# Performance work log

Measured on AMD Instinct MI355X. Metric: run time of the kernel, lower is better.

## Reference

```python
import jax, jax.numpy as jnp
import numpy as np

B, N_HIST, N_PRED = 32, 12, 12
N_NODE, INPUT_DIM, OUTPUT_DIM = 325, 2, 1
HIDDEN, N_RNN_LAYERS = 256, 2
EDGE_DIM, NODE_DIM, ORDER = 2, 64, 2
K = ORDER * EDGE_DIM + 1  # number of concat blocks per GraphConv


def setup_inputs() -> dict:
    key = jax.random.key(0)
    ks = iter(jax.random.split(key, 40))

    def rn(shape, s=0.05):
        return jax.random.normal(next(ks), shape, jnp.float32) * s

    L, H = N_RNN_LAYERS, HIDDEN
    d = {}
    d['inputs'] = jax.random.normal(next(ks), (B, N_HIST, N_NODE, INPUT_DIM), jnp.float32)
    d['vertexes'] = rn((N_NODE, NODE_DIM), 1.0)
    d['arcs_w0'] = rn((2 * NODE_DIM, 4 * NODE_DIM)); d['arcs_b0'] = jnp.zeros((4 * NODE_DIM,), jnp.float32)
    d['arcs_w1'] = rn((4 * NODE_DIM, 4 * NODE_DIM)); d['arcs_b1'] = jnp.zeros((4 * NODE_DIM,), jnp.float32)
    d['arcs_w2'] = rn((4 * NODE_DIM, EDGE_DIM)); d['arcs_b2'] = jnp.zeros((EDGE_DIM,), jnp.float32)
    d['enc_pre_w0'] = rn((K * INPUT_DIM, H)); d['enc_pre_b0'] = jnp.zeros((H,), jnp.float32)
    d['enc_pre_w1'] = rn((K * H, H)); d['enc_pre_b1'] = jnp.zeros((H,), jnp.float32)
    d['enc_wih'] = rn((L, 4 * H, H)); d['enc_whh'] = rn((L, 4 * H, H))
    d['enc_bih'] = jnp.zeros((L, 4 * H), jnp.float32); d['enc_bhh'] = jnp.zeros((L, 4 * H), jnp.float32)
    d['dec_pre_w0'] = rn((K * OUTPUT_DIM, H)); d['dec_pre_b0'] = jnp.zeros((H,), jnp.float32)
    d['dec_pre_w1'] = rn((K * H, H)); d['dec_pre_b1'] = jnp.zeros((H,), jnp.float32)
    d['dec_wih'] = rn((L, 4 * H, H)); d['dec_whh'] = rn((L, 4 * H, H))
    d['dec_bih'] = jnp.zeros((L, 4 * H), jnp.float32); d['dec_bhh'] = jnp.zeros((L, 4 * H), jnp.float32)
    d['dec_post_w0'] = rn((K * H, H)); d['dec_post_b0'] = jnp.zeros((H,), jnp.float32)
    d['dec_post_w1'] = rn((K * H, H)); d['dec_post_b1'] = jnp.zeros((H,), jnp.float32)
    d['proj_w'] = rn((H, OUTPUT_DIM)); d['proj_b'] = jnp.zeros((OUTPUT_DIM,), jnp.float32)
    return d


def _graph_conv(x, supports, w, b):
    out = [x]
    for e in range(supports.shape[0]):
        a = supports[e]
        x1 = x
        for _ in range(ORDER):
            x1 = jnp.einsum('...vc,vw->...wc', x1, a)
            out.append(x1)
    return jnp.concatenate(out, -1) @ w + b


def _stacked_gc(x, supports, layers):
    for w, b in layers:
        x = jax.nn.relu(_graph_conv(x, supports, w, b))
    return x


def _lstm_step(x, h, c, wih, whh, bih, bhh):
    # x: [BN, H]; h, c: [L, BN, H]; torch gate order i, f, g, o
    new_h, new_c = [], []
    for l in range(N_RNN_LAYERS):
        gates = x @ wih[l].T + bih[l] + h[l] @ whh[l].T + bhh[l]
        i, f, g, o = jnp.split(gates, 4, axis=-1)
        cn = jax.nn.sigmoid(f) * c[l] + jax.nn.sigmoid(i) * jnp.tanh(g)
        hn = jax.nn.sigmoid(o) * jnp.tanh(cn)
        new_h.append(hn); new_c.append(cn)
        x = hn
    return x, jnp.stack(new_h), jnp.stack(new_c)


def _adaptive_supports(vertexes, arcs_w0, arcs_b0, arcs_w1, arcs_b1, arcs_w2, arcs_b2):
    n = vertexes.shape[0]
    src = jnp.broadcast_to(vertexes[None, :, :], (n, n, NODE_DIM))
    dst = jnp.broadcast_to(vertexes[:, None, :], (n, n, NODE_DIM))
    h = jnp.concatenate([src, dst], -1)
    h = jax.nn.leaky_relu(h @ arcs_w0 + arcs_b0)
    h = jax.nn.leaky_relu(h @ arcs_w1 + arcs_b1)
    adj = jnp.transpose(h @ arcs_w2 + arcs_b2, (2, 0, 1))  # [E, N, N]
    adj = jax.nn.relu(adj)
    adj = adj / jnp.maximum(jnp.sum(jnp.abs(adj), axis=2, keepdims=True), 1e-12)
    # FAITHFUL to source: adj is computed but the function returns identity.expand(adj.shape)
    return jnp.broadcast_to(jnp.eye(n, dtype=jnp.float32)[None], adj.shape)


def _forward(inputs, vertexes, arcs_w0, arcs_b0, arcs_w1, arcs_b1, arcs_w2, arcs_b2,
             enc_pre_w0, enc_pre_b0, enc_pre_w1, enc_pre_b1,
             enc_wih, enc_whh, enc_bih, enc_bhh,
             dec_pre_w0, dec_pre_b0, dec_pre_w1, dec_pre_b1,
             dec_wih, dec_whh, dec_bih, dec_bhh,
             dec_post_w0, dec_post_b0, dec_post_w1, dec_post_b1,
             proj_w, proj_b):
    b, t, n, _ = inputs.shape
    H, L = HIDDEN, N_RNN_LAYERS
    supports = _adaptive_supports(vertexes, arcs_w0, arcs_b0, arcs_w1, arcs_b1, arcs_w2, arcs_b2)

    # ---- encoding ----
    x = _stacked_gc(inputs, supports, [(enc_pre_w0, enc_pre_b0), (enc_pre_w1, enc_pre_b1)])  # [B,T,N,H]
    seq = jnp.transpose(x, (1, 0, 2, 3)).reshape(t, b * n, H)
    h0 = jnp.zeros((L, b * n, H), inputs.dtype)
    c0 = jnp.zeros((L, b * n, H), inputs.dtype)

    def enc_step(carry, xt):
        hh, cc = carry
        _, hh, cc = _lstm_step(xt, hh, cc, enc_wih, enc_whh, enc_bih, enc_bhh)
        return (hh, cc), None

    (h, c), _ = jax.lax.scan(enc_step, (h0, c0), seq)
    # NOTE: source calls torch.dropout but discards the result -> no-op; reproduced by omission.

    dec_in0 = jnp.zeros((b, n, OUTPUT_DIM), inputs.dtype)
    dec_pre = [(dec_pre_w0, dec_pre_b0), (dec_pre_w1, dec_pre_b1)]
    dec_post = [(dec_post_w0, dec_post_b0), (dec_post_w1, dec_post_b1)]

    def dec_step(carry, _):
        x, hh, cc = carry
        x = _stacked_gc(x, supports, dec_pre)                      # [B,N,H]
        xf, hh, cc = _lstm_step(x.reshape(b * n, H), hh, cc, dec_wih, dec_whh, dec_bih, dec_bhh)
        x = _stacked_gc(xf.reshape(b, n, H), supports, dec_post)   # [B,N,H]
        out = x @ proj_w + proj_b                                  # [B,N,out_dim]
        return (out, hh, cc), out

    _, outs = jax.lax.scan(dec_step, (dec_in0, h, c), None, length=N_PRED)
    return jnp.transpose(outs, (1, 0, 2, 3))  # [B, n_pred, N, output_dim]


def reference(inputs, vertexes, arcs_w0, arcs_b0, arcs_w1, arcs_b1, arcs_w2, arcs_b2,
              enc_pre_w0, enc_pre_b0, enc_pre_w1, enc_pre_b1,
              enc_wih, enc_whh, enc_bih, enc_bhh,
              dec_pre_w0, dec_pre_b0, dec_pre_w1, dec_pre_b1,
              dec_wih, dec_whh, dec_bih, dec_bhh,
              dec_post_w0, dec_post_b0, dec_post_w1, dec_post_b1,
              proj_w, proj_b):
    return _forward(inputs, vertexes, arcs_w0, arcs_b0, arcs_w1, arcs_b1, arcs_w2, arcs_b2,
                    enc_pre_w0, enc_pre_b0, enc_pre_w1, enc_pre_b1,
                    enc_wih, enc_whh, enc_bih, enc_bhh,
                    dec_pre_w0, dec_pre_b0, dec_pre_w1, dec_pre_b1,
                    dec_wih, dec_whh, dec_bih, dec_bhh,
                    dec_post_w0, dec_post_b0, dec_post_w1, dec_post_b1,
                    proj_w, proj_b)
```

## Files before the change

kernel.cpp:

```cpp
#include <hip/hip_runtime.h>
#include <math.h>

#define BATCH 32
#define NNODE 325
#define T_HIST 12
#define T_PRED 12
#define H 256
#define G4 1024
#define ROWS (BATCH*NNODE)
#define MPAD 10496

typedef __attribute__((ext_vector_type(8))) short bf16x8;
typedef __attribute__((ext_vector_type(4))) float f32x4;
typedef unsigned short ushort_t;
typedef unsigned int uint_t;

#define GLL16(gp, sp) __builtin_amdgcn_global_load_lds( \
    (const __attribute__((address_space(1))) void*)(gp), \
    (__attribute__((address_space(3))) void*)(sp), 16, 0, 0)

__device__ inline float bf2f(ushort_t u) { return __uint_as_float(((uint_t)u) << 16); }

__device__ inline void split2(float v, ushort_t& h, ushort_t& l) {
    uint_t b = __float_as_uint(v);
    uint_t hb = (b + 0x7fffu + ((b >> 16) & 1u)) & 0xffff0000u;
    h = (ushort_t)(hb >> 16);
    float r = v - __uint_as_float(hb);
    uint_t rb = __float_as_uint(r);
    l = (ushort_t)((rb + 0x7fffu + ((rb >> 16) & 1u)) >> 16);
}

__device__ inline float sigm(float x) {
    x = fminf(fmaxf(x, -30.f), 30.f);
    return 1.f / (1.f + __expf(-x));
}
__device__ inline float tanh_f(float x) {
    x = fminf(fmaxf(x, -15.f), 15.f);
    float e = __expf(2.f * x);
    return (e - 1.f) / (e + 1.f);
}

__global__ void collapse_kernel(const float* __restrict__ w, float* __restrict__ out,
                                int cin, int nblk) {
    int idx = blockIdx.x * blockDim.x + threadIdx.x;
    if (idx >= cin * H) return;
    int c = idx / H, h = idx % H;
    float s = 0.f;
    for (int k = 0; k < nblk; ++k) s += w[(size_t)(k * cin + c) * H + h];
    out[idx] = s;
}

__global__ void pack_big_kernel(const float* __restrict__ wih, const float* __restrict__ whh,
                                const float* __restrict__ bih, const float* __restrict__ bhh,
                                ushort_t* __restrict__ Bxh, ushort_t* __restrict__ Bxl,
                                ushort_t* __restrict__ Bhh, ushort_t* __restrict__ Bhl,
                                float* __restrict__ biasI) {
    int idx = blockIdx.x * blockDim.x + threadIdx.x;
    if (idx >= 32 * G4) return;
    int kg = idx >> 10, col = idx & 1023;
    int j = col >> 2, g = col & 3;
    int gcol = g * 256 + j;
    if (kg == 0) biasI[col] = bih[gcol] + bhh[gcol];
#pragma unroll
    for (int jj = 0; jj < 8; ++jj) {
        int k = kg * 8 + jj;
        ushort_t hh, ll;
        split2(wih[(size_t)gcol * H + k], hh, ll);
        Bxh[(size_t)idx * 8 + jj] = hh; Bxl[(size_t)idx * 8 + jj] = ll;
        split2(whh[(size_t)gcol * H + k], hh, ll);
        Bhh[(size_t)idx * 8 + jj] = hh; Bhl[(size_t)idx * 8 + jj] = ll;
    }
}

__global__ void pack_small_kernel(const float* __restrict__ w,
                                  ushort_t* __restrict__ Bh, ushort_t* __restrict__ Bl) {
    int idx = blockIdx.x * blockDim.x + threadIdx.x;
    if (idx >= 32 * H) return;
    int kg = idx >> 8, n = idx & 255;
#pragma unroll
    for (int jj = 0; jj < 8; ++jj) {
        int k = kg * 8 + jj;
        float s = 0.f;
        for (int blk = 0; blk < 5; ++blk) s += w[(size_t)(blk * H + k) * H + n];
        ushort_t hh, ll; split2(s, hh, ll);
        Bh[(size_t)idx * 8 + jj] = hh; Bl[(size_t)idx * 8 + jj] = ll;
    }
}

__global__ void enc_pre0_pk(const float* __restrict__ inp, const float* __restrict__ w,
                            const float* __restrict__ b, ushort_t* __restrict__ oh,
                            ushort_t* __restrict__ ol, int t) {
    int m = blockIdx.x * 256 + threadIdx.x;
    int kg = blockIdx.y;
    float ip0 = 0.f, ip1 = 0.f;
    if (m < ROWS) {
        int bb = m / NNODE, nn = m % NNODE;
        const float* ip = inp + (((size_t)bb * T_HIST + t) * NNODE + nn) * 2;
        ip0 = ip[0]; ip1 = ip[1];
    }
    union { ushort_t u[8]; bf16x8 v; } hc, lc;
#pragma unroll
    for (int jj = 0; jj < 8; ++jj) {
        int j = kg * 8 + jj;
        float v = (m < ROWS) ? fmaxf(ip0 * w[j] + ip1 * w[H + j] + b[j], 0.f) : 0.f;
        split2(v, hc.u[jj], lc.u[jj]);
    }
    size_t base = ((size_t)kg * MPAD + m) * 8;
    *(bf16x8*)&oh[base] = hc.v;
    *(bf16x8*)&ol[base] = lc.v;
}

__global__ void dec_pre0_pk(const float* __restrict__ y, const float* __restrict__ w,
                            const float* __restrict__ b, ushort_t* __restrict__ oh,
                            ushort_t* __restrict__ ol) {
    int m = blockIdx.x * 256 + threadIdx.x;
    int kg = blockIdx.y;
    float yv = y[m];
    union { ushort_t u[8]; bf16x8 v; } hc, lc;
#pragma unroll
    for (int jj = 0; jj < 8; ++jj) {
        int j = kg * 8 + jj;
        float v = fmaxf(yv * w[j] + b[j], 0.f);
        split2(v, hc.u[jj], lc.u[jj]);
    }
    size_t base = ((size_t)kg * MPAD + m) * 8;
    *(bf16x8*)&oh[base] = hc.v;
    *(bf16x8*)&ol[base] = lc.v;
}

template<bool GATES, int NSC, int HSC, int BNT, int NBG, bool PRIO>
__device__ __forceinline__ void gemm_body(
    const ushort_t* AxH, const ushort_t* AxL,
    const ushort_t* AhH, const ushort_t* AhL,
    const ushort_t* BxH, const ushort_t* BxL,
    const ushort_t* BhH, const ushort_t* BhL,
    const float* bias, float* cst,
    ushort_t* OH, ushort_t* OL,
    int nbx, int bid)
{
    constexpr int BCH = BNT * 4;
    constexpr int JB  = BNT / 32;
    __shared__ __align__(16) ushort_t As[2][2][4096];
    __shared__ __align__(16) ushort_t Bs[2][2][BCH * 8];

    const int bm = (bid / nbx) * 128, bn = (bid % nbx) * BNT;
    const int tid = threadIdx.x, lane = tid & 63;
    const int wm = (tid >> 7) & 1, wn = (tid >> 6) & 1;
    const int l15 = lane & 15, lk = lane >> 4;

    auto stageSC = [&](int s, int slot) {
        const ushort_t *Ah, *Al, *Bh, *Bl; int ck;
        if (s < HSC) { Ah = AxH; Al = AxL; Bh = BxH; Bl = BxL; ck = s; }
        else         { Ah = AhH; Al = AhL; Bh = BhH; Bl = BhL; ck = s - HSC; }
#pragma unroll
        for (int q = 0; q < 2; ++q) {
            int ubase = (tid & 192) + q * 256;
            int u = ubase + lane;
            int kgl = u >> 7, rc = u & 127;
            size_t ga = ((size_t)(ck * 4 + kgl) * MPAD + bm + rc) * 8;
            GLL16(Ah + ga, &As[slot][0][ubase * 8]);
            GLL16(Al + ga, &As[slot][1][ubase * 8]);
        }
        {
            int ubase = tid & 192;
            int kgl = tid >> 6, nc = tid & 63;
            size_t gb = ((size_t)(ck * 4 + kgl) * NBG + bn + nc) * 8;
            GLL16(Bh + gb, &Bs[slot][0][ubase * 8]);
            GLL16(Bl + gb, &Bs[slot][1][ubase * 8]);
        }
    };

    f32x4 acc[4][JB] = {};

    stageSC(0, 0);

#pragma unroll
    for (int s = 0; s < NSC; ++s) {
        __builtin_amdgcn_s_barrier();
        if (s + 1 < NSC) {
            stageSC(s + 1, (s + 1) & 1);
            asm volatile("s_waitcnt vmcnt(6)" ::: "memory");
        } else {
            asm volatile("s_waitcnt vmcnt(0)" ::: "memory");
        }
        __builtin_amdgcn_s_barrier();
        __builtin_amdgcn_sched_barrier(0);

        const int slot = s & 1;
        bf16x8 ah[4], al[4], bh[JB], bl[JB];
#pragma unroll
        for (int i = 0; i < 4; ++i) {
            int ea = (lk * 128 + wm * 64 + i * 16 + l15) * 8;
            ah[i] = *(const bf16x8*)&As[slot][0][ea];
            al[i] = *(const bf16x8*)&As[slot][1][ea];
        }
#pragma unroll
        for (int j = 0; j < JB; ++j) {
            int eb = (lk * BNT + wn * (BNT / 2) + j * 16 + l15) * 8;
            bh[j] = *(const bf16x8*)&Bs[slot][0][eb];
            bl[j] = *(const bf16x8*)&Bs[slot][1][eb];
        }
        if constexpr (PRIO) __builtin_amdgcn_s_setprio(1);
#pragma unroll
        for (int i = 0; i < 4; ++i)
#pragma unroll
            for (int j = 0; j < JB; ++j)
                acc[i][j] = __builtin_amdgcn_mfma_f32_16x16x32_bf16(bh[j], ah[i], acc[i][j], 0, 0, 0);
#pragma unroll
        for (int i = 0; i < 4; ++i)
#pragma unroll
            for (int j = 0; j < JB; ++j)
                acc[i][j] = __builtin_amdgcn_mfma_f32_16x16x32_bf16(bl[j], ah[i], acc[i][j], 0, 0, 0);
#pragma unroll
        for (int i = 0; i < 4; ++i)
#pragma unroll
            for (int j = 0; j < JB; ++j)
                acc[i][j] = __builtin_amdgcn_mfma_f32_16x16x32_bf16(bh[j], al[i], acc[i][j], 0, 0, 0);
        if constexpr (PRIO) __builtin_amdgcn_s_setprio(0);
    }

    if constexpr (GATES) {
        uint_t* Hs = (uint_t*)&As[0][0][0];
        const int jb0 = (bn >> 2) + wn * 8;
#pragma unroll
        for (int j = 0; j < JB; ++j) {
            float4 b4 = *(const float4*)&bias[bn + wn * 32 + j * 16 + lk * 4];
            int cell = jb0 + j * 4 + lk;
#pragma unroll
            for (int i = 0; i < 4; ++i) {
                int m = bm + wm * 64 + i * 16 + l15;
                float vi = acc[i][j][0] + b4.x;
                float vf = acc[i][j][1] + b4.y;
                float vg = acc[i][j][2] + b4.z;
                float vo = acc[i][j][3] + b4.w;
                size_t ci = (size_t)cell * MPAD + m;
                float cold = cst[ci];
                float cn = sigm(vf) * cold + sigm(vi) * tanh_f(vg);
                float hn = sigm(vo) * tanh_f(cn);
                cst[ci] = cn;
                ushort_t hh, hl; split2(hn, hh, hl);
                Hs[(wm * 64 + i * 16 + l15) * 17 + wn * 8 + j * 4 + lk] = ((uint_t)hh << 16) | hl;
            }
        }
        __syncthreads();
        {
            int mloc = tid & 127, kgl = tid >> 7;
            union { ushort_t u[8]; bf16x8 v; } hi, lo;
#pragma unroll
            for (int jj = 0; jj < 8; ++jj) {
                uint_t wv = Hs[mloc * 17 + kgl * 8 + jj];
                hi.u[jj] = (ushort_t)(wv >> 16);
                lo.u[jj] = (ushort_t)(wv & 0xffffu);
            }
            size_t base = ((size_t)((bn >> 5) + kgl) * MPAD + bm + mloc) * 8;
            *(bf16x8*)&OH[base] = hi.v;
            *(bf16x8*)&OL[base] = lo.v;
        }
    } else {
#pragma unroll
        for (int j = 0; j < JB; ++j) {
            float4 b4 = *(const float4*)&bias[bn + wn * (BNT / 2) + j * 16 + lk * 4];
#pragma unroll
            for (int i = 0; i < 4; ++i) {
                float v0 = fmaxf(acc[i][j][0] + b4.x, 0.f);
                float v1 = fmaxf(acc[i][j][1] + b4.y, 0.f);
                float v2 = fmaxf(acc[i][j][2] + b4.z, 0.f);
                float v3 = fmaxf(acc[i][j][3] + b4.w, 0.f);
                ushort_t h0, h1, h2, h3, l0, l1, l2, l3;
                split2(v0, h0, l0); split2(v1, h1, l1);
                split2(v2, h2, l2); split2(v3, h3, l3);
                uint_t hu0 = (uint_t)h0 | ((uint_t)h1 << 16), hu1 = (uint_t)h2 | ((uint_t)h3 << 16);
                uint_t lu0 = (uint_t)l0 | ((uint_t)l1 << 16), lu1 = (uint_t)l2 | ((uint_t)l3 << 16);
                uint_t ph0 = (uint_t)__shfl_xor((int)hu0, 16, 64);
                uint_t ph1 = (uint_t)__shfl_xor((int)hu1, 16, 64);
                uint_t pl0 = (uint_t)__shfl_xor((int)lu0, 16, 64);
                uint_t pl1 = (uint_t)__shfl_xor((int)lu1, 16, 64);
                int kgg = ((bn + wn * (BNT / 2) + j * 16) >> 3) + (lk >> 1);
                size_t base = ((size_t)kgg * MPAD + bm + wm * 64 + i * 16 + l15) * 8;
                union { uint_t u2[4]; bf16x8 v; } ch;
                if ((lk & 1) == 0) {
                    ch.u2[0] = hu0; ch.u2[1] = hu1; ch.u2[2] = ph0; ch.u2[3] = ph1;
                    *(bf16x8*)&OH[base] = ch.v;
                } else {
                    ch.u2[0] = pl0; ch.u2[1] = pl1; ch.u2[2] = lu0; ch.u2[3] = lu1;
                    *(bf16x8*)&OL[base] = ch.v;
                }
            }
        }
    }
}

struct GArgs {
    const ushort_t *AxH, *AxL, *AhH, *AhL;
    const ushort_t *BxH, *BxL, *BhH, *BhL;
    const float* bias;
    float* cst;
    ushort_t *OH, *OL;
};

template<bool GATES, int NSC, int HSC, int BNT, int NBG, int MINW>
__global__ __launch_bounds__(256, MINW) void gemm_k(
    const ushort_t* __restrict__ AxH, const ushort_t* __restrict__ AxL,
    const ushort_t* __restrict__ AhH, const ushort_t* __restrict__ AhL,
    const ushort_t* __restrict__ BxH, const ushort_t* __restrict__ BxL,
    const ushort_t* __restrict__ BhH, const ushort_t* __restrict__ BhL,
    const float* __restrict__ bias, float* __restrict__ cst,
    ushort_t* __restrict__ OH, ushort_t* __restrict__ OL,
    int nbx, int doSwz)
{
    int bid = blockIdx.x;
    if (doSwz) { int cpx = gridDim.x >> 3; bid = (bid & 7) * cpx + (bid >> 3); }
    gemm_body<GATES, NSC, HSC, BNT, NBG, false>(AxH, AxL, AhH, AhL, BxH, BxL, BhH, BhL,
                                                bias, cst, OH, OL, nbx, bid);
}

__global__ __launch_bounds__(256, 3) void gemm_big_pair(GArgs a, GArgs b, int nblk0) {
    int raw = blockIdx.x;
    int sel = raw >= nblk0;
    int local = sel ? raw - nblk0 : raw;
    int cnt = sel ? (int)gridDim.x - nblk0 : nblk0;
    int cpx = cnt >> 3;
    int bid = (local & 7) * cpx + (local >> 3);
    const ushort_t* AxH = sel ? b.AxH : a.AxH;
    const ushort_t* AxL = sel ? b.AxL : a.AxL;
    const ushort_t* AhH = sel ? b.AhH : a.AhH;
    const ushort_t* AhL = sel ? b.AhL : a.AhL;
    const ushort_t* BxH = sel ? b.BxH : a.BxH;
    const ushort_t* BxL = sel ? b.BxL : a.BxL;
    const ushort_t* BhH = sel ? b.BhH : a.BhH;
    const ushort_t* BhL = sel ? b.BhL : a.BhL;
    const float* bias = sel ? b.bias : a.bias;
    float* cst = sel ? b.cst : a.cst;
    ushort_t* OH = sel ? b.OH : a.OH;
    ushort_t* OL = sel ? b.OL : a.OL;
    gemm_body<true, 16, 8, 64, 1024, true>(AxH, AxL, AhH, AhL, BxH, BxL, BhH, BhL,
                                           bias, cst, OH, OL, 16, bid);
}

__global__ void proj_pre0_kernel(const ushort_t* __restrict__ xh, const ushort_t* __restrict__ xl,
                                 const float* __restrict__ pw, const float* __restrict__ pb,
                                 const float* __restrict__ w, const float* __restrict__ b,
                                 ushort_t* __restrict__ oh, ushort_t* __restrict__ ol,
                                 float* __restrict__ out, int t) {
    int wid = threadIdx.x >> 6, lane = threadIdx.x & 63;
    int r = blockIdx.x * 4 + wid;
    if (r >= ROWS) return;
    const int kg = lane >> 1, sub = (lane & 1) * 4;
    size_t base = ((size_t)kg * MPAD + r) * 8 + sub;
    float s = 0.f;
#pragma unroll
    for (int q = 0; q < 4; ++q) {
        int k = kg * 8 + sub + q;
        s += (bf2f(xh[base + q]) + bf2f(xl[base + q])) * pw[k];
    }
#pragma unroll
    for (int off = 32; off > 0; off >>= 1) s += __shfl_down(s, off, 64);
    float yv = __shfl(s, 0, 64) + pb[0];
    if (lane == 0) {
        int bb = r / NNODE, n = r % NNODE;
        out[((size_t)bb * T_PRED + t) * NNODE + n] = yv;
    }
    union { ushort_t u[4]; uint2 v; } hs, ls;
#pragma unroll
    for (int q = 0; q < 4; ++q) {
        int k = kg * 8 + sub + q;
        float v = fmaxf(yv * w[k] + b[k], 0.f);
        split2(v, hs.u[q], ls.u[q]);
    }
    *(uint2*)&oh[base] = hs.v;
    *(uint2*)&ol[base] = ls.v;
}

static inline GArgs mkargs(const ushort_t* xH, const ushort_t* xL,
                           const ushort_t* hH, const ushort_t* hL,
                           ushort_t* const* B, const float* bias, float* c,
                           ushort_t* oH, ushort_t* oL) {
    GArgs g;
    g.AxH = xH; g.AxL = xL; g.AhH = hH; g.AhL = hL;
    g.BxH = B[0]; g.BxL = B[1]; g.BhH = B[2]; g.BhL = B[3];
    g.bias = bias; g.cst = c; g.OH = oH; g.OL = oL;
    return g;
}
static inline void big_single(const ushort_t* xH, const ushort_t* xL,
                              const ushort_t* hH, const ushort_t* hL,
                              ushort_t* const* B, const float* bias, float* c,
                              ushort_t* oH, ushort_t* oL, hipStream_t s) {
    gemm_k<true, 16, 8, 64, 1024, 3><<<1312, 256, 0, s>>>(
        xH, xL, hH, hL, B[0], B[1], B[2], B[3], bias, c, oH, oL, 16, 1);
}
static inline void big_pair(const GArgs& g0, const GArgs& g1, hipStream_t s) {
    gemm_big_pair<<<2624, 256, 0, s>>>(g0, g1, 1312);
}
static inline void gemm_small(const ushort_t* aH, const ushort_t* aL,
                              const ushort_t* bH, const ushort_t* bL, const float* bias,
                              ushort_t* oH, ushort_t* oL, hipStream_t s) {
    gemm_k<false, 8, 8, 64, 256, 3><<<82 * 4, 256, 0, s>>>(
        aH, aL, aH, aL, bH, bL, bH, bL, bias, nullptr, oH, oL, 4, 1);
}

extern "C" void kernel_launch(void* const* d_in, const int* in_sizes, int n_in,
                              void* d_out, int out_size, void* d_ws, size_t ws_size,
                              hipStream_t stream) {
    (void)in_sizes; (void)n_in; (void)out_size; (void)ws_size;

    const float* inputs      = (const float*)d_in[0];
    const float* enc_pre_w0  = (const float*)d_in[8];
    const float* enc_pre_b0  = (const float*)d_in[9];
    const float* enc_pre_w1  = (const float*)d_in[10];
    const float* enc_pre_b1  = (const float*)d_in[11];
    const float* enc_wih     = (const float*)d_in[12];
    const float* enc_whh     = (const float*)d_in[13];
    const float* enc_bih     = (const float*)d_in[14];
    const float* enc_bhh     = (const float*)d_in[15];
    const float* dec_pre_w0  = (const float*)d_in[16];
    const float* dec_pre_b0  = (const float*)d_in[17];
    const float* dec_pre_w1  = (const float*)d_in[18];
    const float* dec_pre_b1  = (const float*)d_in[19];
    const float* dec_wih     = (const float*)d_in[20];
    const float* dec_whh     = (const float*)d_in[21];
    const float* dec_bih     = (const float*)d_in[22];
    const float* dec_bhh     = (const float*)d_in[23];
    const float* dec_post_w0 = (const float*)d_in[24];
    const float* dec_post_b0 = (const float*)d_in[25];
    const float* dec_post_w1 = (const float*)d_in[26];
    const float* dec_post_b1 = (const float*)d_in[27];
    const float* proj_w      = (const float*)d_in[28];
    const float* proj_b      = (const float*)d_in[29];
    float* out = (float*)d_out;

    char* wsb = (char*)d_ws;
    size_t off = 0;
    auto allocF = [&](size_t n) { float* p = (float*)(wsb + off); off += ((n * 4 + 15) & ~(size_t)15); return p; };
    auto allocU = [&](size_t n) { ushort_t* p = (ushort_t*)(wsb + off); off += ((n * 2 + 15) & ~(size_t)15); return p; };

    const size_t BIGW = (size_t)32 * G4 * 8;
    const size_t SMLW = (size_t)32 * H * 8;
    const size_t ACT  = (size_t)32 * MPAD * 8;

    ushort_t* eB0[4]; ushort_t* eB1[4]; ushort_t* dB0[4]; ushort_t* dB1[4];
    for (int q = 0; q < 4; ++q) eB0[q] = allocU(BIGW);
    for (int q = 0; q < 4; ++q) eB1[q] = allocU(BIGW);
    for (int q = 0; q < 4; ++q) dB0[q] = allocU(BIGW);
    for (int q = 0; q < 4; ++q) dB1[q] = allocU(BIGW);
    float* eBI0 = allocF(G4); float* eBI1 = allocF(G4);
    float* dBI0 = allocF(G4); float* dBI1 = allocF(G4);
    ushort_t* eP1h = allocU(SMLW); ushort_t* eP1l = allocU(SMLW);
    ushort_t* dP1h = allocU(SMLW); ushort_t* dP1l = allocU(SMLW);
    ushort_t* po0h = allocU(SMLW); ushort_t* po0l = allocU(SMLW);
    ushort_t* po1h = allocU(SMLW); ushort_t* po1l = allocU(SMLW);
    float* encW0eff = allocF(2 * H);
    float* decPre0eff = allocF(H);
    ushort_t* h0H[2]; ushort_t* h0L[2]; ushort_t* h1H[2]; ushort_t* h1L[2];
    for (int q = 0; q < 2; ++q) { h0H[q] = allocU(ACT); h0L[q] = allocU(ACT); }
    for (int q = 0; q < 2; ++q) { h1H[q] = allocU(ACT); h1L[q] = allocU(ACT); }
    float* c0 = allocF((size_t)H * MPAD);
    float* c1 = allocF((size_t)H * MPAD);
    ushort_t* xaH = allocU(ACT); ushort_t* xaL = allocU(ACT);
    ushort_t* xbH = allocU(ACT); ushort_t* xbL = allocU(ACT);
    float* y = allocF(MPAD);

    const size_t LOFF = (size_t)G4 * H;
    const int EW = 256;

    pack_big_kernel<<<128, EW, 0, stream>>>(enc_wih, enc_whh, enc_bih, enc_bhh,
                                            eB0[0], eB0[1], eB0[2], eB0[3], eBI0);
    pack_big_kernel<<<128, EW, 0, stream>>>(enc_wih + LOFF, enc_whh + LOFF, enc_bih + G4, enc_bhh + G4,
                                            eB1[0], eB1[1], eB1[2], eB1[3], eBI1);
    pack_big_kernel<<<128, EW, 0, stream>>>(dec_wih, dec_whh, dec_bih, dec_bhh,
                                            dB0[0], dB0[1], dB0[2], dB0[3], dBI0);
    pack_big_kernel<<<128, EW, 0, stream>>>(dec_wih + LOFF, dec_whh + LOFF, dec_bih + G4, dec_bhh + G4,
                                            dB1[0], dB1[1], dB1[2], dB1[3], dBI1);
    pack_small_kernel<<<32, EW, 0, stream>>>(enc_pre_w1, eP1h, eP1l);
    pack_small_kernel<<<32, EW, 0, stream>>>(dec_pre_w1, dP1h, dP1l);
    pack_small_kernel<<<32, EW, 0, stream>>>(dec_post_w0, po0h, po0l);
    pack_small_kernel<<<32, EW, 0, stream>>>(dec_post_w1, po1h, po1l);
    collapse_kernel<<<2, EW, 0, stream>>>(enc_pre_w0, encW0eff, 2, 5);
    collapse_kernel<<<1, EW, 0, stream>>>(dec_pre_w0, decPre0eff, 1, 5);

    for (int q = 0; q < 2; ++q) {
        hipMemsetAsync(h0H[q], 0, ACT * 2, stream); hipMemsetAsync(h0L[q], 0, ACT * 2, stream);
        hipMemsetAsync(h1H[q], 0, ACT * 2, stream); hipMemsetAsync(h1L[q], 0, ACT * 2, stream);
    }
    hipMemsetAsync(c0, 0, (size_t)H * MPAD * 4, stream);
    hipMemsetAsync(c1, 0, (size_t)H * MPAD * 4, stream);
    hipMemsetAsync(y, 0, (size_t)MPAD * 4, stream);

    const dim3 PG(MPAD / 256, 32);

    enc_pre0_pk<<<PG, EW, 0, stream>>>(inputs, encW0eff, enc_pre_b0, xaH, xaL, 0);
    gemm_small(xaH, xaL, eP1h, eP1l, enc_pre_b1, xbH, xbL, stream);
    big_single(xbH, xbL, h0H[0], h0L[0], eB0, eBI0, c0, h0H[1], h0L[1], stream);
    for (int t = 0; t < T_HIST - 1; ++t) {
        int pr = t & 1;
        enc_pre0_pk<<<PG, EW, 0, stream>>>(inputs, encW0eff, enc_pre_b0, xaH, xaL, t + 1);
        gemm_small(xaH, xaL, eP1h, eP1l, enc_pre_b1, xbH, xbL, stream);
        GArgs gL1 = mkargs(h0H[pr ^ 1], h0L[pr ^ 1], h1H[pr], h1L[pr],
                           eB1, eBI1, c1, h1H[pr ^ 1], h1L[pr ^ 1]);
        GArgs gL0 = mkargs(xbH, xbL, h0H[pr ^ 1], h0L[pr ^ 1],
                           eB0, eBI0, c0, h0H[pr], h0L[pr]);
        big_pair(gL1, gL0, stream);
    }
    big_single(h0H[0], h0L[0], h1H[1], h1L[1], eB1, eBI1, c1, h1H[0], h1L[0], stream);

    dec_pre0_pk<<<PG, EW, 0, stream>>>(y, decPre0eff, dec_pre_b0, xaH, xaL);
    for (int d = 0; d < T_PRED; ++d) {
        int pr = d & 1;
        gemm_small(xaH, xaL, dP1h, dP1l, dec_pre_b1, xbH, xbL, stream);
        big_single(xbH, xbL, h0H[pr], h0L[pr], dB0, dBI0, c0,
                   h0H[pr ^ 1], h0L[pr ^ 1], stream);
        big_single(h0H[pr ^ 1], h0L[pr ^ 1], h1H[pr], h1L[pr], dB1, dBI1, c1,
                   h1H[pr ^ 1], h1L[pr ^ 1], stream);
        gemm_small(h1H[pr ^ 1], h1L[pr ^ 1], po0h, po0l, dec_post_b0, xaH, xaL, stream);
        gemm_small(xaH, xaL, po1h, po1l, dec_post_b1, xbH, xbL, stream);
        proj_pre0_kernel<<<(ROWS + 3) / 4, EW, 0, stream>>>(
            xbH, xbL, proj_w, proj_b, decPre0eff, dec_pre_b0, xaH, xaL, out, d);
    }
}
```

Baseline: 2.381 ms.

## Fold next-step encoder input GEMM into the paired LSTM gate kernel

The encoder input GraphConv small GEMM for step t+2 is now computed inside the same launch as the paired layer-0/layer-1 LSTM gate GEMMs. Its blocks are appended to the grid and the input buffers are double-buffered so the result is ready in time. This removes one kernel launch per encoder step and lets the small GEMM fill idle CUs alongside the large ones. The cost is extra double buffers and a fixed, hardcoded block partition in the combined kernel.

```diff
diff --git a/kernel.cpp b/kernel.cpp
--- a/kernel.cpp
+++ b/kernel.cpp
@@ -314,27 +314,23 @@
                                                 bias, cst, OH, OL, nbx, bid);
 }
 
-__global__ __launch_bounds__(256, 3) void gemm_big_pair(GArgs a, GArgs b, int nblk0) {
+__global__ __launch_bounds__(256, 3) void gemm_pair3(GArgs a, GArgs b, GArgs sm) {
     int raw = blockIdx.x;
-    int sel = raw >= nblk0;
-    int local = sel ? raw - nblk0 : raw;
-    int cnt = sel ? (int)gridDim.x - nblk0 : nblk0;
-    int cpx = cnt >> 3;
-    int bid = (local & 7) * cpx + (local >> 3);
-    const ushort_t* AxH = sel ? b.AxH : a.AxH;
-    const ushort_t* AxL = sel ? b.AxL : a.AxL;
-    const ushort_t* AhH = sel ? b.AhH : a.AhH;
-    const ushort_t* AhL = sel ? b.AhL : a.AhL;
-    const ushort_t* BxH = sel ? b.BxH : a.BxH;
-    const ushort_t* BxL = sel ? b.BxL : a.BxL;
-    const ushort_t* BhH = sel ? b.BhH : a.BhH;
-    const ushort_t* BhL = sel ? b.BhL : a.BhL;
-    const float* bias = sel ? b.bias : a.bias;
-    float* cst = sel ? b.cst : a.cst;
-    ushort_t* OH = sel ? b.OH : a.OH;
-    ushort_t* OL = sel ? b.OL : a.OL;
-    gemm_body<true, 16, 8, 64, 1024, true>(AxH, AxL, AhH, AhL, BxH, BxL, BhH, BhL,
-                                           bias, cst, OH, OL, 16, bid);
+    if (raw < 2624) {
+        int sel = raw >= 1312;
+        int local = sel ? raw - 1312 : raw;
+        int bid = (local & 7) * 164 + (local >> 3);
+        const GArgs& g = sel ? b : a;
+        gemm_body<true, 16, 8, 64, 1024, true>(g.AxH, g.AxL, g.AhH, g.AhL,
+                                               g.BxH, g.BxL, g.BhH, g.BhL,
+                                               g.bias, g.cst, g.OH, g.OL, 16, bid);
+    } else {
+        int local = raw - 2624;
+        int bid = (local & 7) * 41 + (local >> 3);
+        gemm_body<false, 8, 8, 64, 256, true>(sm.AxH, sm.AxL, sm.AhH, sm.AhL,
+                                              sm.BxH, sm.BxL, sm.BhH, sm.BhL,
+                                              sm.bias, sm.cst, sm.OH, sm.OL, 4, bid);
+    }
 }
 
 __global__ void proj_pre0_kernel(const ushort_t* __restrict__ xh, const ushort_t* __restrict__ xl,
@@ -381,15 +377,21 @@
     g.bias = bias; g.cst = c; g.OH = oH; g.OL = oL;
     return g;
 }
+static inline GArgs mkargs_small(const ushort_t* aH, const ushort_t* aL,
+                                 const ushort_t* bH, const ushort_t* bL,
+                                 const float* bias, ushort_t* oH, ushort_t* oL) {
+    GArgs g;
+    g.AxH = aH; g.AxL = aL; g.AhH = aH; g.AhL = aL;
+    g.BxH = bH; g.BxL = bL; g.BhH = bH; g.BhL = bL;
+    g.bias = bias; g.cst = nullptr; g.OH = oH; g.OL = oL;
+    return g;
+}
 static inline void big_single(const ushort_t* xH, const ushort_t* xL,
                               const ushort_t* hH, const ushort_t* hL,
                               ushort_t* const* B, const float* bias, float* c,
                               ushort_t* oH, ushort_t* oL, hipStream_t s) {
     gemm_k<true, 16, 8, 64, 1024, 3><<<1312, 256, 0, s>>>(
         xH, xL, hH, hL, B[0], B[1], B[2], B[3], bias, c, oH, oL, 16, 1);
-}
-static inline void big_pair(const GArgs& g0, const GArgs& g1, hipStream_t s) {
-    gemm_big_pair<<<2624, 256, 0, s>>>(g0, g1, 1312);
 }
 static inline void gemm_small(const ushort_t* aH, const ushort_t* aL,
                               const ushort_t* bH, const ushort_t* bL, const float* bias,
@@ -455,8 +457,9 @@
     for (int q = 0; q < 2; ++q) { h1H[q] = allocU(ACT); h1L[q] = allocU(ACT); }
     float* c0 = allocF((size_t)H * MPAD);
     float* c1 = allocF((size_t)H * MPAD);
-    ushort_t* xaH = allocU(ACT); ushort_t* xaL = allocU(ACT);
-    ushort_t* xbH = allocU(ACT); ushort_t* xbL = allocU(ACT);
+    ushort_t* xaH[2]; ushort_t* xaL[2]; ushort_t* xbH[2]; ushort_t* xbL[2];
+    for (int q = 0; q < 2; ++q) { xaH[q] = allocU(ACT); xaL[q] = allocU(ACT); }
+    for (int q = 0; q < 2; ++q) { xbH[q] = allocU(ACT); xbL[q] = allocU(ACT); }
     float* y = allocF(MPAD);
 
     const size_t LOFF = (size_t)G4 * H;
@@ -487,32 +490,40 @@
 
     const dim3 PG(MPAD / 256, 32);
 
-    enc_pre0_pk<<<PG, EW, 0, stream>>>(inputs, encW0eff, enc_pre_b0, xaH, xaL, 0);
-    gemm_small(xaH, xaL, eP1h, eP1l, enc_pre_b1, xbH, xbL, stream);
-    big_single(xbH, xbL, h0H[0], h0L[0], eB0, eBI0, c0, h0H[1], h0L[1], stream);
+    enc_pre0_pk<<<PG, EW, 0, stream>>>(inputs, encW0eff, enc_pre_b0, xaH[0], xaL[0], 0);
+    gemm_small(xaH[0], xaL[0], eP1h, eP1l, enc_pre_b1, xbH[0], xbL[0], stream);
+    enc_pre0_pk<<<PG, EW, 0, stream>>>(inputs, encW0eff, enc_pre_b0, xaH[1], xaL[1], 1);
+    gemm_small(xaH[1], xaL[1], eP1h, eP1l, enc_pre_b1, xbH[1], xbL[1], stream);
+    big_single(xbH[0], xbL[0], h0H[0], h0L[0], eB0, eBI0, c0, h0H[1], h0L[1], stream);
     for (int t = 0; t < T_HIST - 1; ++t) {
         int pr = t & 1;
-        enc_pre0_pk<<<PG, EW, 0, stream>>>(inputs, encW0eff, enc_pre_b0, xaH, xaL, t + 1);
-        gemm_small(xaH, xaL, eP1h, eP1l, enc_pre_b1, xbH, xbL, stream);
         GArgs gL1 = mkargs(h0H[pr ^ 1], h0L[pr ^ 1], h1H[pr], h1L[pr],
                            eB1, eBI1, c1, h1H[pr ^ 1], h1L[pr ^ 1]);
-        GArgs gL0 = mkargs(xbH, xbL, h0H[pr ^ 1], h0L[pr ^ 1],
+        GArgs gL0 = mkargs(xbH[pr ^ 1], xbL[pr ^ 1], h0H[pr ^ 1], h0L[pr ^ 1],
                            eB0, eBI0, c0, h0H[pr], h0L[pr]);
-        big_pair(gL1, gL0, stream);
+        if (t + 2 <= T_HIST - 1) {
+            enc_pre0_pk<<<PG, EW, 0, stream>>>(inputs, encW0eff, enc_pre_b0,
+                                               xaH[pr], xaL[pr], t + 2);
+            GArgs gSm = mkargs_small(xaH[pr], xaL[pr], eP1h, eP1l, enc_pre_b1,
+                                     xbH[pr], xbL[pr]);
+            gemm_pair3<<<2952, 256, 0, stream>>>(gL1, gL0, gSm);
+        } else {
+            gemm_pair3<<<2624, 256, 0, stream>>>(gL1, gL0, gL0 );
+        }
     }
     big_single(h0H[0], h0L[0], h1H[1], h1L[1], eB1, eBI1, c1, h1H[0], h1L[0], stream);
 
-    dec_pre0_pk<<<PG, EW, 0, stream>>>(y, decPre0eff, dec_pre_b0, xaH, xaL);
+    dec_pre0_pk<<<PG, EW, 0, stream>>>(y, decPre0eff, dec_pre_b0, xaH[0], xaL[0]);
     for (int d = 0; d < T_PRED; ++d) {
         int pr = d & 1;
-        gemm_small(xaH, xaL, dP1h, dP1l, dec_pre_b1, xbH, xbL, stream);
-        big_single(xbH, xbL, h0H[pr], h0L[pr], dB0, dBI0, c0,
+        gemm_small(xaH[0], xaL[0], dP1h, dP1l, dec_pre_b1, xbH[0], xbL[0], stream);
+        big_single(xbH[0], xbL[0], h0H[pr], h0L[pr], dB0, dBI0, c0,
                    h0H[pr ^ 1], h0L[pr ^ 1], stream);
         big_single(h0H[pr ^ 1], h0L[pr ^ 1], h1H[pr], h1L[pr], dB1, dBI1, c1,
                    h1H[pr ^ 1], h1L[pr ^ 1], stream);
-        gemm_small(h1H[pr ^ 1], h1L[pr ^ 1], po0h, po0l, dec_post_b0, xaH, xaL, stream);
-        gemm_small(xaH, xaL, po1h, po1l, dec_post_b1, xbH, xbL, stream);
+        gemm_small(h1H[pr ^ 1], h1L[pr ^ 1], po0h, po0l, dec_post_b0, xaH[0], xaL[0], stream);
+        gemm_small(xaH[0], xaL[0], po1h, po1l, dec_post_b1, xbH[0], xbL[0], stream);
         proj_pre0_kernel<<<(ROWS + 3) / 4, EW, 0, stream>>>(
-            xbH, xbL, proj_w, proj_b, decPre0eff, dec_pre_b0, xaH, xaL, out, d);
-    }
-}
+            xbH[0], xbL[0], proj_w, proj_b, decPre0eff, dec_pre_b0, xaH[0], xaL[0], out, d);
+    }
+}
```

After: 2.927 ms. 22.9% more time.
